# Kernel optimization log

Hardware: AMD Instinct MI355X
Metric: run time of the kernel (lower is better)

Reference implementation:

```python
import math
import jax, jax.numpy as jnp
import numpy as np

D_MODEL = 1024
N_HEADS = 16
HEAD_DIM = D_MODEL // N_HEADS
D_FF = 4096
LN_EPS = 1e-5


def _layer_norm(x, g, b):
    mu = jnp.mean(x, axis=-1, keepdims=True)
    var = jnp.var(x, axis=-1, keepdims=True)
    return (x - mu) * jax.lax.rsqrt(var + LN_EPS) * g + b


def setup_inputs() -> dict:
    key = jax.random.key(0)
    ks = jax.random.split(key, 8)
    s = 0.02
    d, dff = D_MODEL, D_FF
    return {
        "src": jax.random.normal(ks[0], (2, 2048, d), dtype=jnp.float32),
        "in_proj_w": jax.random.normal(ks[1], (3 * d, d), dtype=jnp.float32) * s,
        "in_proj_b": jnp.zeros((3 * d,), dtype=jnp.float32),
        "out_w": jax.random.normal(ks[2], (d, d), dtype=jnp.float32) * s,
        "out_b": jnp.zeros((d,), dtype=jnp.float32),
        "lin1_w": jax.random.normal(ks[3], (dff, d), dtype=jnp.float32) * s,
        "lin1_b": jnp.zeros((dff,), dtype=jnp.float32),
        "lin2_w": jax.random.normal(ks[4], (d, dff), dtype=jnp.float32) * s,
        "lin2_b": jnp.zeros((d,), dtype=jnp.float32),
        "ln1_g": jnp.ones((d,), dtype=jnp.float32),
        "ln1_b": jnp.zeros((d,), dtype=jnp.float32),
        "ln2_g": jnp.ones((d,), dtype=jnp.float32),
        "ln2_b": jnp.zeros((d,), dtype=jnp.float32),
    }


def reference(src, in_proj_w, in_proj_b, out_w, out_b, lin1_w, lin1_b,
              lin2_w, lin2_b, ln1_g, ln1_b, ln2_g, ln2_b):
    B, S, d = src.shape
    # QKV projections (in_proj_weight split at d, then kv split)
    q = src @ in_proj_w[:d].T + in_proj_b[:d]              # [B,S,d]
    kv = src @ in_proj_w[d:].T + in_proj_b[d:]             # [B,S,2d]
    q = q.reshape(B, S, N_HEADS, HEAD_DIM)
    kv = kv.reshape(B, S, 2, N_HEADS, HEAD_DIM)
    k, v = kv[:, :, 0], kv[:, :, 1]
    softmax_scale = 1.0 / math.sqrt(HEAD_DIM)
    scores = jnp.einsum('bthd,bshd->bhts', q, k) * softmax_scale  # [B,H,Sq,Skv]
    # 'distribute': softmax over the QUERY dimension (dim=-2)
    attention = jax.nn.softmax(scores, axis=-2)
    post = jnp.einsum('bhts,bshd->bthd', attention, v)     # [B,Sq,H,hd]
    # post-attention activation 'gelu' (torch exact gelu)
    post = jax.nn.gelu(post, approximate=False)
    # attention_scale == 'sqrt': divide by sqrt(kv_len)
    post = post / math.sqrt(S)
    attn_out = post.reshape(B, S, d) @ out_w.T + out_b
    # post-norm residual structure (pre_norm=False, dropout=0)
    x = _layer_norm(src + attn_out, ln1_g, ln1_b)
    ff = jax.nn.gelu(x @ lin1_w.T + lin1_b, approximate=False) @ lin2_w.T + lin2_b
    return _layer_norm(x + ff, ln2_g, ln2_b)
```

## Files before the change

### kernel.cpp

```cpp
#include <hip/hip_runtime.h>
#include <hip/hip_bf16.h>
#include <math.h>


using bf16x8 = __attribute__((ext_vector_type(8))) short;
using f32x4  = __attribute__((ext_vector_type(4))) float;

__device__ inline f32x4 mfma16(bf16x8 a, bf16x8 b, f32x4 c) {
    return __builtin_amdgcn_mfma_f32_16x16x32_bf16(a, b, c, 0, 0, 0);
}

__device__ inline ushort f2bf(float f) {
    union { float f; unsigned u; } x; x.f = f;
    unsigned r = x.u + 0x7fffu + ((x.u >> 16) & 1u);
    return (ushort)(r >> 16);
}

__device__ inline float bf2f(ushort u) {
    union { unsigned u; float f; } x; x.u = ((unsigned)u) << 16; return x.f;
}

__device__ inline unsigned pk2bf(float a, float b) {
    __hip_bfloat162 h = __float22bfloat162_rn(float2{a, b});
    union { __hip_bfloat162 h; unsigned u; } x; x.h = h;
    return x.u;
}

__device__ inline float gelu_fast(float v) {
    float u = v * (1.5957691216f + 0.0713548162f * v * v);
    float e = __expf(u);
    return v * (e / (e + 1.0f));
}

__device__ __forceinline__ void gl2lds16(const ushort* g, ushort* l) {
    __builtin_amdgcn_global_load_lds(
        (const __attribute__((address_space(1))) unsigned int*)g,
        (__attribute__((address_space(3))) unsigned int*)l,
        16, 0, 0);
}

__global__ __launch_bounds__(256) void cvt_all(const float4* __restrict__ s0,
                                               const float4* __restrict__ s1,
                                               const float4* __restrict__ s2,
                                               const float4* __restrict__ s3,
                                               const float4* __restrict__ s4,
                                               ushort4* __restrict__ out) {
    int i = blockIdx.x * 256 + threadIdx.x;
    const float4* p;
    int off;
    if (i < 1048576)      { p = s0; off = i; }
    else if (i < 1835008) { p = s1; off = i - 1048576; }
    else if (i < 2097152) { p = s2; off = i - 1835008; }
    else if (i < 3145728) { p = s3; off = i - 2097152; }
    else                  { p = s4; off = i - 3145728; }
    float4 v = p[off];
    ushort4 o;
    o.x = f2bf(v.x); o.y = f2bf(v.y); o.z = f2bf(v.z); o.w = f2bf(v.w);
    out[i] = o;
}

__global__ __launch_bounds__(256) void gemm_bt(
    const ushort* __restrict__ A, const ushort* __restrict__ Bw,
    const float* __restrict__ bias, int M, int N, int K, int kLen, int mode, int gx,
    ushort* __restrict__ ob0, ushort* __restrict__ ob1, ushort* __restrict__ ob2) {
    __shared__ ushort As[2][128 * 32];
    __shared__ ushort Bs[2][128 * 32];
    int tid = threadIdx.x, lane = tid & 63, w = tid >> 6;
    int wm = w >> 1, wn = w & 1;

    int Nx = gridDim.x, Ny = gridDim.y;
    int bx = blockIdx.x, by = blockIdx.y;
    int gy = 8 / gx;
    if ((Nx % gx) == 0 && (Ny % gy) == 0 && ((Nx * Ny) & 7) == 0) {
        int Sx = Nx / gx, Sy = Ny / gy;
        int i = bx + Nx * by;
        int c = i & 7, j = i >> 3;
        int cx = c % gx, cy = c / gx;
        bx = cx * Sx + j % Sx;
        by = cy * Sy + (j / Sx) % Sy;
    }
    int bm = by * 128, bn = bx * 128;
    int kz = blockIdx.z;
    int q4 = lane >> 4, l15 = lane & 15;
    f32x4 acc[4][4] = {};

    int srow = w * 16 + (lane >> 2);
    int scg = lane & 3;
    const ushort* Ab = A + (size_t)bm * K + (size_t)kz * kLen;
    const ushort* Bb = Bw + (size_t)bn * K + (size_t)kz * kLen;
    const ushort* gA0 = Ab + (size_t)srow * K + scg * 8;
    const ushort* gA1 = Ab + (size_t)(64 + srow) * K + scg * 8;
    const ushort* gB0 = Bb + (size_t)srow * K + scg * 8;
    const ushort* gB1 = Bb + (size_t)(64 + srow) * K + scg * 8;
    ushort* lA00 = As[0] + w * 512;
    ushort* lA10 = As[0] + 2048 + w * 512;
    ushort* lB00 = Bs[0] + w * 512;
    ushort* lB10 = Bs[0] + 2048 + w * 512;
    ushort* lA01 = As[1] + w * 512;
    ushort* lA11 = As[1] + 2048 + w * 512;
    ushort* lB01 = Bs[1] + w * 512;
    ushort* lB11 = Bs[1] + 2048 + w * 512;

    const ushort* aB[2] = { &As[0][(wm * 64 + l15) * 32 + q4 * 8],
                            &As[1][(wm * 64 + l15) * 32 + q4 * 8] };
    const ushort* bB[2] = { &Bs[0][(wn * 64 + l15) * 32 + q4 * 8],
                            &Bs[1][(wn * 64 + l15) * 32 + q4 * 8] };

    for (int k0 = 0; k0 < kLen; k0 += 64) {
        __syncthreads();
        gl2lds16(gA0 + k0, lA00);
        gl2lds16(gA1 + k0, lA10);
        gl2lds16(gB0 + k0, lB00);
        gl2lds16(gB1 + k0, lB10);
        gl2lds16(gA0 + k0 + 32, lA01);
        gl2lds16(gA1 + k0 + 32, lA11);
        gl2lds16(gB0 + k0 + 32, lB01);
        gl2lds16(gB1 + k0 + 32, lB11);
        __syncthreads();
#pragma unroll
        for (int u = 0; u < 2; u++) {
            bf16x8 af[4], bfr[4];
#pragma unroll
            for (int mi = 0; mi < 4; mi++)
                af[mi] = *(const bf16x8*)(aB[u] + mi * 512);
#pragma unroll
            for (int ni = 0; ni < 4; ni++)
                bfr[ni] = *(const bf16x8*)(bB[u] + ni * 512);
#pragma unroll
            for (int mi = 0; mi < 4; mi++)
#pragma unroll
                for (int ni = 0; ni < 4; ni++)
                    acc[mi][ni] = mfma16(af[mi], bfr[ni], acc[mi][ni]);
        }
    }

    int r0 = bm + wm * 64, c0 = bn + wn * 64;
#pragma unroll
    for (int mi = 0; mi < 4; mi++) {
#pragma unroll
        for (int ni = 0; ni < 4; ni++) {
            int colg = c0 + ni * 16 + l15;
            float bv = (mode == 3) ? 0.f : bias[colg];
#pragma unroll
            for (int r = 0; r < 4; r++) {
                int rowg = r0 + mi * 16 + q4 * 4 + r;
                float v = acc[mi][ni][r] + bv;
                if (mode == 0) {
                    if (colg < 1024) {
                        ob0[(size_t)rowg * 1024 + colg] = f2bf(v);
                    } else if (colg < 2048) {
                        ob1[(size_t)rowg * 1024 + (colg - 1024)] = f2bf(v);
                    } else {
                        ob2[(size_t)rowg * 1024 + (colg - 2048)] = f2bf(v);
                    }
                } else if (mode == 2) {
                    ob0[(size_t)rowg * N + colg] = f2bf(gelu_fast(v));
                } else {
                    ob0[(size_t)kz * M * N + (size_t)rowg * N + colg] = f2bf(v);
                }
            }
        }
    }
}

__global__ __launch_bounds__(256) void attn_colsum_foldv(const ushort* __restrict__ qb,
                                                         const ushort* __restrict__ kb,
                                                         const ushort* __restrict__ vrow,
                                                         ushort* __restrict__ vt) {
    __shared__ ushort Qs[64 * 72];
    __shared__ float NinvS[128];
    int tid = threadIdx.x, lane = tid & 63, w = tid >> 6;
    int bh = blockIdx.x >> 4, sblk = blockIdx.x & 15;
    int b = bh >> 4, h = bh & 15;
    int q4 = lane >> 4, l15 = lane & 15;
    const ushort* qbase = qb + (size_t)(b * 2048) * 1024 + h * 64;
    const ushort* kbase = kb + (size_t)(b * 2048) * 1024 + h * 64;
    int s_base = sblk * 128 + w * 32;

    bf16x8 ka[2][2];
#pragma unroll
    for (int mi = 0; mi < 2; mi++) {
        const ushort* kp = kbase + (size_t)(s_base + mi * 16 + l15) * 1024 + q4 * 8;
        ka[mi][0] = *(const bf16x8*)(kp);
        ka[mi][1] = *(const bf16x8*)(kp + 32);
    }
    float acc[2][4] = {};

    int rl = lane >> 3;
    int cswz = (((lane & 7) ^ rl) << 3);
    int swf = l15 & 7;
    int c0s = (q4 ^ swf) << 3;
    int c1s = ((q4 + 4) ^ swf) << 3;
    for (int t0 = 0; t0 < 2048; t0 += 64) {
        __syncthreads();
        gl2lds16(qbase + (size_t)(t0 + w * 16 + rl) * 1024 + cswz, Qs + (w * 16) * 64);
        gl2lds16(qbase + (size_t)(t0 + w * 16 + 8 + rl) * 1024 + cswz, Qs + (w * 16 + 8) * 64);
        __syncthreads();
#pragma unroll
        for (int tsub = 0; tsub < 4; tsub++) {
            int rQ = (tsub * 16 + l15) * 64;
            bf16x8 bq0 = *(const bf16x8*)&Qs[rQ + c0s];
            bf16x8 bq1 = *(const bf16x8*)&Qs[rQ + c1s];
#pragma unroll
            for (int mi = 0; mi < 2; mi++) {
                f32x4 d = {0.f, 0.f, 0.f, 0.f};
                d = mfma16(ka[mi][0], bq0, d);
                d = mfma16(ka[mi][1], bq1, d);
#pragma unroll
                for (int r = 0; r < 4; r++)
                    acc[mi][r] += __expf(d[r] * 0.125f);
            }
        }
    }
#pragma unroll
    for (int mi = 0; mi < 2; mi++)
#pragma unroll
        for (int r = 0; r < 4; r++) {
            float v = acc[mi][r];
            v += __shfl_xor(v, 1); v += __shfl_xor(v, 2);
            v += __shfl_xor(v, 4); v += __shfl_xor(v, 8);
            if (l15 == 0)
                NinvS[w * 32 + mi * 16 + q4 * 4 + r] = 1.f / v;
        }

    int sl = tid >> 3, dh8 = (tid & 7) * 8;
#pragma unroll
    for (int batch = 0; batch < 2; batch++) {
        int bs = sblk * 128 + batch * 64;
        __syncthreads();
#pragma unroll
        for (int rep = 0; rep < 2; rep++) {
            int s = sl + rep * 32;
            float n = NinvS[batch * 64 + s];
            const ushort* p = vrow + (size_t)(b * 2048 + bs + s) * 1024 + h * 64 + dh8;
            ushort4 u0 = ((const ushort4*)p)[0];
            ushort4 u1 = ((const ushort4*)p)[1];
            ushort4 o0, o1;
            o0.x = f2bf(bf2f(u0.x) * n); o0.y = f2bf(bf2f(u0.y) * n);
            o0.z = f2bf(bf2f(u0.z) * n); o0.w = f2bf(bf2f(u0.w) * n);
            o1.x = f2bf(bf2f(u1.x) * n); o1.y = f2bf(bf2f(u1.y) * n);
            o1.z = f2bf(bf2f(u1.z) * n); o1.w = f2bf(bf2f(u1.w) * n);
            *(ushort4*)&Qs[s * 72 + dh8] = o0;
            *(ushort4*)&Qs[s * 72 + dh8 + 4] = o1;
        }
        __syncthreads();
        int dhl = tid >> 3, soff = (tid & 7) * 8;
#pragma unroll
        for (int rep = 0; rep < 2; rep++) {
            int d = dhl + rep * 32;
            ushort tmp[8];
#pragma unroll
            for (int j = 0; j < 8; j++) tmp[j] = Qs[(soff + j) * 72 + d];
            *(uint4*)(vt + ((size_t)bh * 64 + d) * 2048 + bs + soff) = *(uint4*)tmp;
        }
    }
}

__global__ __launch_bounds__(256) void attn_pv(const ushort* __restrict__ qb,
                                               const ushort* __restrict__ kb,
                                               const ushort* __restrict__ vt,
                                               ushort* __restrict__ post) {
    __shared__ ushort Ks[64 * 64];
    __shared__ ushort Vs[64 * 64];
    __shared__ ushort Ps[4][32 * 68];
    int tid = threadIdx.x, lane = tid & 63, w = tid >> 6;
    int bh = blockIdx.x >> 4, tblk = blockIdx.x & 15;
    int b = bh >> 4, h = bh & 15;
    int q4 = lane >> 4, l15 = lane & 15;
    const ushort* qbase = qb + (size_t)(b * 2048) * 1024 + h * 64;
    const ushort* kbase = kb + (size_t)(b * 2048) * 1024 + h * 64;
    const ushort* vtb = vt + (size_t)bh * 64 * 2048;
    int t_base = tblk * 128 + w * 32;

    bf16x8 aq[2][2];
#pragma unroll
    for (int mi = 0; mi < 2; mi++) {
        const ushort* qp = qbase + (size_t)(t_base + mi * 16 + l15) * 1024 + q4 * 8;
        aq[mi][0] = *(const bf16x8*)(qp);
        aq[mi][1] = *(const bf16x8*)(qp + 32);
    }
    f32x4 oacc[2][4] = {};
    ushort* myP = Ps[w];

    int rl = lane >> 3;
    int cswz = (((lane & 7) ^ rl) << 3);
    int swf = l15 & 7;
    int c0s = (q4 ^ swf) << 3;
    int c1s = ((q4 + 4) ^ swf) << 3;
    for (int s0 = 0; s0 < 2048; s0 += 64) {
        __syncthreads();
        gl2lds16(kbase + (size_t)(s0 + w * 16 + rl) * 1024 + cswz, Ks + (w * 16) * 64);
        gl2lds16(kbase + (size_t)(s0 + w * 16 + 8 + rl) * 1024 + cswz, Ks + (w * 16 + 8) * 64);
        gl2lds16(vtb + (size_t)(w * 16 + rl) * 2048 + s0 + cswz, Vs + (w * 16) * 64);
        gl2lds16(vtb + (size_t)(w * 16 + 8 + rl) * 2048 + s0 + cswz, Vs + (w * 16 + 8) * 64);
        __syncthreads();
#pragma unroll
        for (int ssub = 0; ssub < 4; ssub++) {
            int rA = (ssub * 16 + l15) * 64;
            bf16x8 bk0 = *(const bf16x8*)&Ks[rA + c0s];
            bf16x8 bk1 = *(const bf16x8*)&Ks[rA + c1s];
#pragma unroll
            for (int mi = 0; mi < 2; mi++) {
                f32x4 d = {0.f, 0.f, 0.f, 0.f};
                d = mfma16(bk0, aq[mi][0], d);
                d = mfma16(bk1, aq[mi][1], d);
                float p0 = __expf(d[0] * 0.125f);
                float p1 = __expf(d[1] * 0.125f);
                float p2 = __expf(d[2] * 0.125f);
                float p3 = __expf(d[3] * 0.125f);
                uint2 uu;
                uu.x = pk2bf(p0, p1);
                uu.y = pk2bf(p2, p3);
                *(uint2*)&myP[(mi * 16 + l15) * 68 + ssub * 16 + q4 * 4] = uu;
            }
        }
#pragma unroll
        for (int mi = 0; mi < 2; mi++) {
            bf16x8 ap0 = *(const bf16x8*)&myP[(mi * 16 + l15) * 68 + q4 * 8];
            bf16x8 ap1 = *(const bf16x8*)&myP[(mi * 16 + l15) * 68 + 32 + q4 * 8];
#pragma unroll
            for (int ni = 0; ni < 4; ni++) {
                int rV = (ni * 16 + l15) * 64;
                bf16x8 bv0 = *(const bf16x8*)&Vs[rV + c0s];
                bf16x8 bv1 = *(const bf16x8*)&Vs[rV + c1s];
                oacc[mi][ni] = mfma16(ap0, bv0, oacc[mi][ni]);
                oacc[mi][ni] = mfma16(ap1, bv1, oacc[mi][ni]);
            }
        }
    }
#pragma unroll
    for (int mi = 0; mi < 2; mi++)
#pragma unroll
        for (int ni = 0; ni < 4; ni++)
#pragma unroll
            for (int r = 0; r < 4; r++) {
                int t = t_base + mi * 16 + q4 * 4 + r;
                float g = gelu_fast(oacc[mi][ni][r]) * 0.022097086912079608f;
                post[(size_t)(b * 2048 + t) * 1024 + h * 64 + ni * 16 + l15] = f2bf(g);
            }
}

__global__ __launch_bounds__(256) void ln_comb4(const ushort* __restrict__ parts,
                                                const float* __restrict__ bias,
                                                const float* __restrict__ res,
                                                const float* __restrict__ gw,
                                                const float* __restrict__ bw,
                                                ushort* __restrict__ outb,
                                                float* __restrict__ outf) {
    const size_t PLANE = (size_t)4096 * 1024;
    int row = blockIdx.x, tid = threadIdx.x;
    int lane = tid & 63, wid = tid >> 6;
    size_t off = (size_t)row * 1024 + tid * 4;
    float4 r = *(const float4*)(res + off);
    float4 bb = *(const float4*)(bias + tid * 4);
    float4 v;
    v.x = r.x + bb.x; v.y = r.y + bb.y; v.z = r.z + bb.z; v.w = r.w + bb.w;
#pragma unroll
    for (int p = 0; p < 4; p++) {
        ushort4 u = *(const ushort4*)(parts + p * PLANE + off);
        v.x += bf2f(u.x); v.y += bf2f(u.y); v.z += bf2f(u.z); v.w += bf2f(u.w);
    }
    float s = v.x + v.y + v.z + v.w;
    float ss = v.x * v.x + v.y * v.y + v.z * v.z + v.w * v.w;
    for (int m = 1; m < 64; m <<= 1) { s += __shfl_xor(s, m); ss += __shfl_xor(ss, m); }
    __shared__ float red[8];
    if (lane == 0) { red[wid] = s; red[wid + 4] = ss; }
    __syncthreads();
    s = red[0] + red[1] + red[2] + red[3];
    ss = red[4] + red[5] + red[6] + red[7];
    float mu = s * (1.f / 1024.f);
    float var = ss * (1.f / 1024.f) - mu * mu;
    float inv = rsqrtf(var + 1e-5f);
    float4 gv = *(const float4*)(gw + tid * 4);
    float4 bv = *(const float4*)(bw + tid * 4);
    float o0 = (v.x - mu) * inv * gv.x + bv.x;
    float o1 = (v.y - mu) * inv * gv.y + bv.y;
    float o2 = (v.z - mu) * inv * gv.z + bv.z;
    float o3 = (v.w - mu) * inv * gv.w + bv.w;
    if (outf) {
        float4 o; o.x = o0; o.y = o1; o.z = o2; o.w = o3;
        *(float4*)(outf + off) = o;
    }
    if (outb) {
        ushort4 o; o.x = f2bf(o0); o.y = f2bf(o1); o.z = f2bf(o2); o.w = f2bf(o3);
        *(ushort4*)(outb + off) = o;
    }
}

extern "C" void kernel_launch(void* const* d_in, const int* in_sizes, int n_in,
                              void* d_out, int out_size, void* d_ws, size_t ws_size,
                              hipStream_t stream) {
    const float* src  = (const float*)d_in[0];
    const float* w_in = (const float*)d_in[1];
    const float* b_in = (const float*)d_in[2];
    const float* w_o  = (const float*)d_in[3];
    const float* b_o  = (const float*)d_in[4];
    const float* w1   = (const float*)d_in[5];
    const float* b1   = (const float*)d_in[6];
    const float* w2   = (const float*)d_in[7];
    const float* b2   = (const float*)d_in[8];
    const float* g1   = (const float*)d_in[9];
    const float* be1  = (const float*)d_in[10];
    const float* g2   = (const float*)d_in[11];
    const float* be2  = (const float*)d_in[12];
    float* out = (float*)d_out;

    const size_t M = 4096;
    char* wsp = (char*)d_ws;
    size_t off = 0;
    auto alloc = [&](size_t bytes) -> void* {
        void* p = wsp + off;
        off = (off + bytes + 255) & ~(size_t)255;
        return p;
    };
    ushort* src_bf  = (ushort*)alloc(M * 1024 * 2);
    ushort* win_bf  = (ushort*)alloc(3072 * 1024 * 2);
    ushort* wout_bf = (ushort*)alloc(1024 * 1024 * 2);
    ushort* w1_bf   = (ushort*)alloc(4096 * 1024 * 2);
    ushort* w2_bf   = (ushort*)alloc((size_t)1024 * 4096 * 2);
    ushort* q_bf    = (ushort*)alloc(M * 1024 * 2);
    ushort* k_bf    = (ushort*)alloc(M * 1024 * 2);
    ushort* vt_bf   = (ushort*)alloc(M * 1024 * 2);
    ushort* post_bf = (ushort*)alloc(M * 1024 * 2);
    ushort* part    = (ushort*)alloc(4 * M * 1024 * 2);
    ushort* x_bf    = (ushort*)alloc(M * 1024 * 2);
    float*  x_f32   = (float*)alloc(M * 1024 * 4);
    ushort* h1_bf   = (ushort*)alloc(M * 4096 * 2);
    ushort* v_row   = part;

    cvt_all<<<16384, 256, 0, stream>>>((const float4*)src, (const float4*)w_in,
                                       (const float4*)w_o, (const float4*)w1,
                                       (const float4*)w2, (ushort4*)src_bf);

    gemm_bt<<<dim3(24, 32, 1), 256, 0, stream>>>(src_bf, win_bf, b_in, 4096, 3072, 1024, 1024, 0, 2,
                                                 q_bf, k_bf, v_row);

    attn_colsum_foldv<<<512, 256, 0, stream>>>(q_bf, k_bf, v_row, vt_bf);
    attn_pv<<<512, 256, 0, stream>>>(q_bf, k_bf, vt_bf, post_bf);

    gemm_bt<<<dim3(8, 32, 4), 256, 0, stream>>>(post_bf, wout_bf, b_o, 4096, 1024, 1024, 256, 3, 1,
                                                part, nullptr, nullptr);
    ln_comb4<<<4096, 256, 0, stream>>>(part, b_o, src, g1, be1, x_bf, x_f32);

    gemm_bt<<<dim3(32, 32, 1), 256, 0, stream>>>(x_bf, w1_bf, b1, 4096, 4096, 1024, 1024, 2, 2,
                                                 h1_bf, nullptr, nullptr);
    gemm_bt<<<dim3(8, 32, 4), 256, 0, stream>>>(h1_bf, w2_bf, b2, 4096, 1024, 4096, 1024, 3, 1,
                                                part, nullptr, nullptr);
    ln_comb4<<<4096, 256, 0, stream>>>(part, b2, x_f32, g2, be2, nullptr, out);
}
```

Measured before the change: 469.9 us.

## Split attention reductions over key/query halves to double grid parallelism

```diff
diff --git a/kernel.cpp b/kernel.cpp
--- a/kernel.cpp
+++ b/kernel.cpp
@@ -163,14 +163,13 @@
     }
 }
 
-__global__ __launch_bounds__(256) void attn_colsum_foldv(const ushort* __restrict__ qb,
-                                                         const ushort* __restrict__ kb,
-                                                         const ushort* __restrict__ vrow,
-                                                         ushort* __restrict__ vt) {
-    __shared__ ushort Qs[64 * 72];
-    __shared__ float NinvS[128];
+__global__ __launch_bounds__(256) void attn_colsum_part(const ushort* __restrict__ qb,
+                                                        const ushort* __restrict__ kb,
+                                                        float* __restrict__ csum) {
+    __shared__ ushort Qs[64 * 64];
     int tid = threadIdx.x, lane = tid & 63, w = tid >> 6;
-    int bh = blockIdx.x >> 4, sblk = blockIdx.x & 15;
+    int id = blockIdx.x;
+    int th = id & 1, sblk = (id >> 1) & 15, bh = id >> 5;
     int b = bh >> 4, h = bh & 15;
     int q4 = lane >> 4, l15 = lane & 15;
     const ushort* qbase = qb + (size_t)(b * 2048) * 1024 + h * 64;
@@ -191,7 +190,8 @@
     int swf = l15 & 7;
     int c0s = (q4 ^ swf) << 3;
     int c1s = ((q4 + 4) ^ swf) << 3;
-    for (int t0 = 0; t0 < 2048; t0 += 64) {
+    int tEnd = th * 1024 + 1024;
+    for (int t0 = th * 1024; t0 < tEnd; t0 += 64) {
         __syncthreads();
         gl2lds16(qbase + (size_t)(t0 + w * 16 + rl) * 1024 + cswz, Qs + (w * 16) * 64);
         gl2lds16(qbase + (size_t)(t0 + w * 16 + 8 + rl) * 1024 + cswz, Qs + (w * 16 + 8) * 64);
@@ -220,51 +220,57 @@
             v += __shfl_xor(v, 1); v += __shfl_xor(v, 2);
             v += __shfl_xor(v, 4); v += __shfl_xor(v, 8);
             if (l15 == 0)
-                NinvS[w * 32 + mi * 16 + q4 * 4 + r] = 1.f / v;
-        }
-
+                csum[(size_t)th * 65536 + (size_t)bh * 2048 + s_base + mi * 16 + q4 * 4 + r] = v;
+        }
+}
+
+__global__ __launch_bounds__(256) void foldv(const ushort* __restrict__ vrow,
+                                             const float* __restrict__ csum,
+                                             ushort* __restrict__ vt) {
+    __shared__ ushort T[64 * 72];
+    int tid = threadIdx.x;
+    int bh = blockIdx.x >> 5, sch = blockIdx.x & 31;
+    int b = bh >> 4, h = bh & 15;
+    int s0 = sch * 64;
     int sl = tid >> 3, dh8 = (tid & 7) * 8;
 #pragma unroll
-    for (int batch = 0; batch < 2; batch++) {
-        int bs = sblk * 128 + batch * 64;
-        __syncthreads();
-#pragma unroll
-        for (int rep = 0; rep < 2; rep++) {
-            int s = sl + rep * 32;
-            float n = NinvS[batch * 64 + s];
-            const ushort* p = vrow + (size_t)(b * 2048 + bs + s) * 1024 + h * 64 + dh8;
-            ushort4 u0 = ((const ushort4*)p)[0];
-            ushort4 u1 = ((const ushort4*)p)[1];
-            ushort4 o0, o1;
-            o0.x = f2bf(bf2f(u0.x) * n); o0.y = f2bf(bf2f(u0.y) * n);
-            o0.z = f2bf(bf2f(u0.z) * n); o0.w = f2bf(bf2f(u0.w) * n);
-            o1.x = f2bf(bf2f(u1.x) * n); o1.y = f2bf(bf2f(u1.y) * n);
-            o1.z = f2bf(bf2f(u1.z) * n); o1.w = f2bf(bf2f(u1.w) * n);
-            *(ushort4*)&Qs[s * 72 + dh8] = o0;
-            *(ushort4*)&Qs[s * 72 + dh8 + 4] = o1;
-        }
-        __syncthreads();
-        int dhl = tid >> 3, soff = (tid & 7) * 8;
-#pragma unroll
-        for (int rep = 0; rep < 2; rep++) {
-            int d = dhl + rep * 32;
-            ushort tmp[8];
-#pragma unroll
-            for (int j = 0; j < 8; j++) tmp[j] = Qs[(soff + j) * 72 + d];
-            *(uint4*)(vt + ((size_t)bh * 64 + d) * 2048 + bs + soff) = *(uint4*)tmp;
-        }
-    }
-}
-
-__global__ __launch_bounds__(256) void attn_pv(const ushort* __restrict__ qb,
-                                               const ushort* __restrict__ kb,
-                                               const ushort* __restrict__ vt,
-                                               ushort* __restrict__ post) {
+    for (int rep = 0; rep < 2; rep++) {
+        int s = sl + rep * 32;
+        size_t ci = (size_t)bh * 2048 + s0 + s;
+        float n = 1.f / (csum[ci] + csum[65536 + ci]);
+        const ushort* p = vrow + (size_t)(b * 2048 + s0 + s) * 1024 + h * 64 + dh8;
+        ushort4 u0 = ((const ushort4*)p)[0];
+        ushort4 u1 = ((const ushort4*)p)[1];
+        ushort4 o0, o1;
+        o0.x = f2bf(bf2f(u0.x) * n); o0.y = f2bf(bf2f(u0.y) * n);
+        o0.z = f2bf(bf2f(u0.z) * n); o0.w = f2bf(bf2f(u0.w) * n);
+        o1.x = f2bf(bf2f(u1.x) * n); o1.y = f2bf(bf2f(u1.y) * n);
+        o1.z = f2bf(bf2f(u1.z) * n); o1.w = f2bf(bf2f(u1.w) * n);
+        *(ushort4*)&T[s * 72 + dh8] = o0;
+        *(ushort4*)&T[s * 72 + dh8 + 4] = o1;
+    }
+    __syncthreads();
+    int dhl = tid >> 3, soff = (tid & 7) * 8;
+#pragma unroll
+    for (int rep = 0; rep < 2; rep++) {
+        int d = dhl + rep * 32;
+        ushort tmp[8];
+#pragma unroll
+        for (int j = 0; j < 8; j++) tmp[j] = T[(soff + j) * 72 + d];
+        *(uint4*)(vt + ((size_t)bh * 64 + d) * 2048 + s0 + soff) = *(uint4*)tmp;
+    }
+}
+
+__global__ __launch_bounds__(256) void attn_pv_split(const ushort* __restrict__ qb,
+                                                     const ushort* __restrict__ kb,
+                                                     const ushort* __restrict__ vt,
+                                                     ushort* __restrict__ opart) {
     __shared__ ushort Ks[64 * 64];
     __shared__ ushort Vs[64 * 64];
     __shared__ ushort Ps[4][32 * 68];
     int tid = threadIdx.x, lane = tid & 63, w = tid >> 6;
-    int bh = blockIdx.x >> 4, tblk = blockIdx.x & 15;
+    int id = blockIdx.x;
+    int sh = id & 1, tblk = (id >> 1) & 15, bh = id >> 5;
     int b = bh >> 4, h = bh & 15;
     int q4 = lane >> 4, l15 = lane & 15;
     const ushort* qbase = qb + (size_t)(b * 2048) * 1024 + h * 64;
@@ -287,7 +293,8 @@
     int swf = l15 & 7;
     int c0s = (q4 ^ swf) << 3;
     int c1s = ((q4 + 4) ^ swf) << 3;
-    for (int s0 = 0; s0 < 2048; s0 += 64) {
+    int sEnd = sh * 1024 + 1024;
+    for (int s0 = sh * 1024; s0 < sEnd; s0 += 64) {
         __syncthreads();
         gl2lds16(kbase + (size_t)(s0 + w * 16 + rl) * 1024 + cswz, Ks + (w * 16) * 64);
         gl2lds16(kbase + (size_t)(s0 + w * 16 + 8 + rl) * 1024 + cswz, Ks + (w * 16 + 8) * 64);
@@ -328,6 +335,7 @@
             }
         }
     }
+    ushort* op = opart + (size_t)sh * 4096 * 1024;
 #pragma unroll
     for (int mi = 0; mi < 2; mi++)
 #pragma unroll
@@ -335,9 +343,31 @@
 #pragma unroll
             for (int r = 0; r < 4; r++) {
                 int t = t_base + mi * 16 + q4 * 4 + r;
-                float g = gelu_fast(oacc[mi][ni][r]) * 0.022097086912079608f;
-                post[(size_t)(b * 2048 + t) * 1024 + h * 64 + ni * 16 + l15] = f2bf(g);
+                op[(size_t)(b * 2048 + t) * 1024 + h * 64 + ni * 16 + l15] =
+                    f2bf(oacc[mi][ni][r]);
             }
+}
+
+__global__ __launch_bounds__(256) void attn_combine(const ushort* __restrict__ opart,
+                                                    ushort* __restrict__ post) {
+    const size_t PLANE = (size_t)4096 * 1024;
+    size_t base = ((size_t)blockIdx.x * 256 + threadIdx.x) * 8;
+    ushort4 a0 = *(const ushort4*)(opart + base);
+    ushort4 a1 = *(const ushort4*)(opart + base + 4);
+    ushort4 b0 = *(const ushort4*)(opart + PLANE + base);
+    ushort4 b1 = *(const ushort4*)(opart + PLANE + base + 4);
+    const float sc = 0.022097086912079608f;
+    ushort4 o0, o1;
+    o0.x = f2bf(gelu_fast(bf2f(a0.x) + bf2f(b0.x)) * sc);
+    o0.y = f2bf(gelu_fast(bf2f(a0.y) + bf2f(b0.y)) * sc);
+    o0.z = f2bf(gelu_fast(bf2f(a0.z) + bf2f(b0.z)) * sc);
+    o0.w = f2bf(gelu_fast(bf2f(a0.w) + bf2f(b0.w)) * sc);
+    o1.x = f2bf(gelu_fast(bf2f(a1.x) + bf2f(b1.x)) * sc);
+    o1.y = f2bf(gelu_fast(bf2f(a1.y) + bf2f(b1.y)) * sc);
+    o1.z = f2bf(gelu_fast(bf2f(a1.z) + bf2f(b1.z)) * sc);
+    o1.w = f2bf(gelu_fast(bf2f(a1.w) + bf2f(b1.w)) * sc);
+    *(ushort4*)(post + base) = o0;
+    *(ushort4*)(post + base + 4) = o1;
 }
 
 __global__ __launch_bounds__(256) void ln_comb4(const ushort* __restrict__ parts,
@@ -423,10 +453,12 @@
     ushort* vt_bf   = (ushort*)alloc(M * 1024 * 2);
     ushort* post_bf = (ushort*)alloc(M * 1024 * 2);
     ushort* part    = (ushort*)alloc(4 * M * 1024 * 2);
+    float*  csum    = (float*)alloc(2 * 32 * 2048 * 4);
     ushort* x_bf    = (ushort*)alloc(M * 1024 * 2);
     float*  x_f32   = (float*)alloc(M * 1024 * 4);
     ushort* h1_bf   = (ushort*)alloc(M * 4096 * 2);
     ushort* v_row   = part;
+    ushort* opart   = part + M * 1024;
 
     cvt_all<<<16384, 256, 0, stream>>>((const float4*)src, (const float4*)w_in,
                                        (const float4*)w_o, (const float4*)w1,
@@ -435,8 +467,10 @@
     gemm_bt<<<dim3(24, 32, 1), 256, 0, stream>>>(src_bf, win_bf, b_in, 4096, 3072, 1024, 1024, 0, 2,
                                                  q_bf, k_bf, v_row);
 
-    attn_colsum_foldv<<<512, 256, 0, stream>>>(q_bf, k_bf, v_row, vt_bf);
-    attn_pv<<<512, 256, 0, stream>>>(q_bf, k_bf, vt_bf, post_bf);
+    attn_colsum_part<<<1024, 256, 0, stream>>>(q_bf, k_bf, csum);
+    foldv<<<1024, 256, 0, stream>>>(v_row, csum, vt_bf);
+    attn_pv_split<<<1024, 256, 0, stream>>>(q_bf, k_bf, vt_bf, opart);
+    attn_combine<<<2048, 256, 0, stream>>>(opart, post_bf);
 
     gemm_bt<<<dim3(8, 32, 4), 256, 0, stream>>>(post_bf, wout_bf, b_o, 4096, 1024, 1024, 256, 3, 1,
                                                 part, nullptr, nullptr);
```

Measured after the change: 465.8 us. About the same (-0.9%).
